# Kernel optimization log

Hardware: AMD Instinct MI355X
Metric: run time of the kernel (lower is better)

Reference implementation:

```python
import jax, jax.numpy as jnp
import numpy as np

B, S, E, H = 2, 2048, 1024, 16
D = E // H  # head_dim = 64


def setup_inputs() -> dict:
    key = jax.random.key(0)
    ks = jax.random.split(key, 6)
    sc = 0.02
    return {
        "hidden_states": jax.random.normal(ks[0], (B, S, E), dtype=jnp.float32),
        "attn_bias": jax.random.normal(ks[1], (S, S), dtype=jnp.float32) * sc,
        "Wqkv": jax.random.normal(ks[2], (E, 3 * E), dtype=jnp.float32) * sc,
        "bqkv": jax.random.normal(ks[3], (3 * E,), dtype=jnp.float32) * sc,
        "Wproj": jax.random.normal(ks[4], (E, E), dtype=jnp.float32) * sc,
        "bproj": jax.random.normal(ks[5], (E,), dtype=jnp.float32) * sc,
    }


def reference(hidden_states, attn_bias, Wqkv, bqkv, Wproj, bproj):
    b, s, e = hidden_states.shape
    qkv = hidden_states @ Wqkv + bqkv                      # [b,s,3e]
    q, k, v = jnp.split(qkv, 3, axis=-1)                   # each [b,s,e]
    cache_key, cache_value = k, v                          # kvCache
    # [b,h,s,d]
    qh = q.reshape(b, s, H, D).transpose(0, 2, 1, 3)
    kh = k.reshape(b, s, H, D).transpose(0, 2, 1, 3)
    vh = v.reshape(b, s, H, D).transpose(0, 2, 1, 3)
    scores = jnp.einsum("bhqd,bhkd->bhqk", qh, kh) / jnp.sqrt(jnp.float32(D))
    scores = scores + attn_bias[:s, :s][None, None]        # learned additive bias
    causal = jnp.tril(jnp.ones((s, s), dtype=bool))
    scores = jnp.where(causal[None, None], scores, jnp.float32(-1e9))
    attn = jax.nn.softmax(scores, axis=-1)
    ctx = jnp.einsum("bhqk,bhkd->bhqd", attn, vh)
    ctx = ctx.transpose(0, 2, 1, 3).reshape(b, s, e)
    out = ctx @ Wproj + bproj                              # resid dropout p=0 -> identity
    return (out, cache_key, cache_value)
```

## Files before the change

kernel.cpp:

```cpp
#include <hip/hip_runtime.h>

#define B_ 2
#define S_ 2048
#define E_ 1024
#define H_ 16
#define D_ 64

typedef short  s16x8 __attribute__((ext_vector_type(8)));
typedef float  f32x4 __attribute__((ext_vector_type(4)));
typedef unsigned short u16x4 __attribute__((ext_vector_type(4)));

__device__ __forceinline__ ushort f2bf(float f) {
    union { float f; unsigned u; } x; x.f = f;
    unsigned u = x.u + 0x7fffu + ((x.u >> 16) & 1u);
    return (ushort)(u >> 16);
}

__device__ __forceinline__ float fast_exp2(float x) {
    float r; asm("v_exp_f32 %0, %1" : "=v"(r) : "v"(x)); return r;
}

__global__ __launch_bounds__(256) void prep_fused_kernel(
    const float* __restrict__ X, ushort* __restrict__ Xbf,
    const float* __restrict__ Wqkv, ushort* __restrict__ Wqkvt,
    const float* __restrict__ Wproj, ushort* __restrict__ Wprojt)
{
    __shared__ float tile[64][65];
    int blk = blockIdx.x;
    int tid = threadIdx.x;
    if (blk < 4096) {
        int i = (blk * 256 + tid) * 4;
        float4 v = *(const float4*)&X[i];
        u16x4 o;
        o.x = f2bf(v.x); o.y = f2bf(v.y); o.z = f2bf(v.z); o.w = f2bf(v.w);
        *(u16x4*)&Xbf[i] = o;
        return;
    }
    const float* W; ushort* Wt; int Ndim, nb;
    if (blk < 4096 + 768) { blk -= 4096; W = Wqkv;  Wt = Wqkvt;  Ndim = 3 * E_; nb = 48; }
    else                  { blk -= 4864; W = Wproj; Wt = Wprojt; Ndim = E_;     nb = 16; }
    int n0 = (blk % nb) * 64, k0 = (blk / nb) * 64;
    int c = tid & 63;
#pragma unroll
    for (int r = tid >> 6; r < 64; r += 4)
        tile[r][c] = W[(size_t)(k0 + r) * Ndim + n0 + c];
    __syncthreads();
#pragma unroll
    for (int r = tid >> 6; r < 64; r += 4)
        Wt[(size_t)(n0 + r) * E_ + k0 + c] = f2bf(tile[c][r]);
}

__global__ __launch_bounds__(256) void prep_bias_kernel(
    const float* __restrict__ bias, ushort* __restrict__ biasT)
{
    int L = blockIdx.x;
    int qi = (int)((sqrtf(8.0f * (float)L + 1.0f) - 1.0f) * 0.5f);
    while ((qi + 1) * (qi + 2) / 2 <= L) qi++;
    while (qi * (qi + 1) / 2 > L) qi--;
    int ki = L - qi * (qi + 1) / 2;
    int tid = threadIdx.x;
    int w = tid >> 6, quad = (tid >> 4) & 3, l15 = tid & 15;
    const float LOG2E = 1.4426950408889634f;
    s16x8 h0 = (s16x8){0,0,0,0,0,0,0,0}, h1 = (s16x8){0,0,0,0,0,0,0,0};
#pragma unroll
    for (int r = 0; r < 4; r++)
#pragma unroll
        for (int kt = 0; kt < 4; kt++) {
            float v = bias[(size_t)(qi * 64 + w * 16 + quad * 4 + r) * S_
                           + ki * 64 + kt * 16 + l15] * LOG2E;
            ushort u = f2bf(v);
            int idx = r * 4 + kt;
            if (idx < 8) h0[idx] = (short)u; else h1[idx - 8] = (short)u;
        }
    ushort* dst = &biasT[((size_t)L * 256 + tid) * 16];
    *(s16x8*)dst = h0;
    *(s16x8*)(dst + 8) = h1;
}

__global__ __launch_bounds__(256) void gemm_mfma_bt(
    const ushort* __restrict__ A,
    const ushort* __restrict__ Bt,
    const float* __restrict__ bias,
    int M, int N, int K,
    float* __restrict__ C0,
    ushort* __restrict__ Qbf, float* __restrict__ Kf32, ushort* __restrict__ Kbf,
    float* __restrict__ Vf32, int mode)
{
    __shared__ ushort As[128 * 64];
    __shared__ ushort Bs[128 * 64];
    int tid = threadIdx.x;
    int wid = tid >> 6, lane = tid & 63;
    int l15 = lane & 15, quad = lane >> 4;
    int wm = wid >> 1, wn = wid & 1;
    int row0 = blockIdx.y * 128, col0 = blockIdx.x * 128;

    int srow = tid >> 3;
    int pk = (tid & 7) * 8;
    int sk = (((tid & 7) ^ (srow & 7)) * 8);

    f32x4 acc[4][4];
#pragma unroll
    for (int mt = 0; mt < 4; mt++)
#pragma unroll
        for (int nt = 0; nt < 4; nt++) acc[mt][nt] = (f32x4){0.f, 0.f, 0.f, 0.f};

    for (int k0 = 0; k0 < K; k0 += 64) {
        __syncthreads();
#pragma unroll
        for (int c = 0; c < 4; c++) {
            int r = c * 32 + srow;
            __builtin_amdgcn_global_load_lds(
                (const __attribute__((address_space(1))) unsigned int*)
                    &A[(size_t)(row0 + r) * K + k0 + sk],
                (__attribute__((address_space(3))) unsigned int*)&As[r * 64 + pk],
                16, 0, 0);
            __builtin_amdgcn_global_load_lds(
                (const __attribute__((address_space(1))) unsigned int*)
                    &Bt[(size_t)(col0 + r) * K + k0 + sk],
                (__attribute__((address_space(3))) unsigned int*)&Bs[r * 64 + pk],
                16, 0, 0);
        }
        __syncthreads();

#pragma unroll
        for (int kk = 0; kk < 2; kk++) {
            int xc = (((kk * 4 + quad) ^ (l15 & 7)) * 8);
            s16x8 af[4], bf[4];
#pragma unroll
            for (int mt = 0; mt < 4; mt++)
                af[mt] = *(const s16x8*)&As[(wm * 64 + mt * 16 + l15) * 64 + xc];
#pragma unroll
            for (int nt = 0; nt < 4; nt++)
                bf[nt] = *(const s16x8*)&Bs[(wn * 64 + nt * 16 + l15) * 64 + xc];
#pragma unroll
            for (int mt = 0; mt < 4; mt++)
#pragma unroll
                for (int nt = 0; nt < 4; nt++)
                    acc[mt][nt] = __builtin_amdgcn_mfma_f32_16x16x32_bf16(
                        af[mt], bf[nt], acc[mt][nt], 0, 0, 0);
        }
    }

#pragma unroll
    for (int nt = 0; nt < 4; nt++) {
        int n = col0 + wn * 64 + nt * 16 + l15;
        float bv = bias[n];
        if (mode == 1) {
            int seg = n >> 10;
            int nn = n & (E_ - 1);
#pragma unroll
            for (int mt = 0; mt < 4; mt++)
#pragma unroll
                for (int r = 0; r < 4; r++) {
                    int row = row0 + wm * 64 + mt * 16 + quad * 4 + r;
                    float v = acc[mt][nt][r] + bv;
                    size_t idx = (size_t)row * E_ + nn;
                    if (seg == 0)      Qbf[idx] = f2bf(v);
                    else if (seg == 1) { Kf32[idx] = v; Kbf[idx] = f2bf(v); }
                    else               Vf32[idx] = v;
                }
        } else {
#pragma unroll
            for (int mt = 0; mt < 4; mt++)
#pragma unroll
                for (int r = 0; r < 4; r++) {
                    int row = row0 + wm * 64 + mt * 16 + quad * 4 + r;
                    C0[(size_t)row * N + n] = acc[mt][nt][r] + bv;
                }
        }
    }
}

__global__ __launch_bounds__(256) void vtrans_kernel(
    const float* __restrict__ V, ushort* __restrict__ Vt)
{
    __shared__ float tile[64][65];
    int blk = blockIdx.x;
    int s0 = (blk & 31) * 64;
    int bh = blk >> 5;
    int b = bh >> 4, h = bh & 15;
    int tid = threadIdx.x;
    int d = tid & 63;
#pragma unroll
    for (int i = tid >> 6; i < 64; i += 4)
        tile[i][d] = V[((size_t)(b * S_ + s0 + i)) * E_ + h * 64 + d];
    __syncthreads();
    int lane = tid & 63, w = tid >> 6;
    int src = ((lane & 3) * 16) + (lane >> 2);
#pragma unroll
    for (int dd = w; dd < 64; dd += 4)
        Vt[((size_t)(bh * 64 + dd)) * S_ + s0 + lane] = f2bf(tile[src][dd]);
}

__global__ __launch_bounds__(256) void attn_mfma_kernel(
    const ushort* __restrict__ Qbf,
    const ushort* __restrict__ Kbf,
    const ushort* __restrict__ Vt,
    const ushort* __restrict__ biasT,
    ushort* __restrict__ Ctx)
{
    __shared__ ushort Ks[64][64];
    __shared__ ushort Vs[64][64];
    __shared__ ushort Ps[4][16][72];

    int blk = blockIdx.x;
    int bh = blk & 31;
    int pr = blk >> 5;
    int b = bh >> 4, h = bh & 15;
    int tid = threadIdx.x;
    int wid = tid >> 6, lane = tid & 63;
    int l15 = lane & 15, quad = lane >> 4;

    int skey = tid >> 2;
    int scol = (tid & 3) * 16;
    int sc0 = ((((tid & 3) * 2) ^ (skey & 7)) * 8);
    int sc1 = sc0 ^ 8;
    const float scale_l2e = 0.18033688011112042f;

    const size_t krow = (size_t)(b * S_ + skey) * E_ + h * 64 + scol;
    const size_t vrow = (size_t)(bh * 64 + skey) * S_ + scol;
    int rc0 = (quad ^ (l15 & 7)) * 8;

    for (int half = 0; half < 2; half++) {
        int qt = half ? pr : (31 - pr);
        int q0w = qt * 64 + wid * 16;

        const size_t qbase = ((size_t)(b * S_ + q0w + l15)) * E_ + h * 64 + quad * 8;
        s16x8 qa0 = *(const s16x8*)&Qbf[qbase];
        s16x8 qa1 = *(const s16x8*)&Qbf[qbase + 32];

        f32x4 o[4];
#pragma unroll
        for (int dt = 0; dt < 4; dt++) o[dt] = (f32x4){0.f, 0.f, 0.f, 0.f};
        float lsum[4];
#pragma unroll
        for (int r = 0; r < 4; r++) lsum[r] = 0.f;

        float4 kr0 = ((const float4*)&Kbf[krow])[0];
        float4 kr1 = ((const float4*)&Kbf[krow])[1];
        float4 vr0 = ((const float4*)&Vt[vrow])[0];
        float4 vr1 = ((const float4*)&Vt[vrow])[1];
        const ushort* bt = &biasT[((size_t)(qt * (qt + 1) / 2) * 256 + tid) * 16];
        s16x8 bn0 = *(const s16x8*)bt;
        s16x8 bn1 = *(const s16x8*)(bt + 8);

        for (int t = 0; t <= qt; t++) {
            int j0 = t * 64;
            __syncthreads();
            *(float4*)&Ks[skey][sc0] = kr0;
            *(float4*)&Ks[skey][sc1] = kr1;
            *(float4*)&Vs[skey][sc0] = vr0;
            *(float4*)&Vs[skey][sc1] = vr1;
            s16x8 b0 = bn0, b1 = bn1;
            __syncthreads();

            if (t < qt) {
                int j1 = j0 + 64;
                kr0 = ((const float4*)&Kbf[krow + (size_t)j1 * E_])[0];
                kr1 = ((const float4*)&Kbf[krow + (size_t)j1 * E_])[1];
                vr0 = ((const float4*)&Vt[vrow + j1])[0];
                vr1 = ((const float4*)&Vt[vrow + j1])[1];
                const ushort* btn = bt + (size_t)(t + 1) * 4096;
                bn0 = *(const s16x8*)btn;
                bn1 = *(const s16x8*)(btn + 8);
            }

            f32x4 s[4];
#pragma unroll
            for (int kt = 0; kt < 4; kt++) {
                s16x8 kb0 = *(const s16x8*)&Ks[kt * 16 + l15][rc0];
                s16x8 kb1 = *(const s16x8*)&Ks[kt * 16 + l15][rc0 ^ 32];
                f32x4 acc = (f32x4){0.f, 0.f, 0.f, 0.f};
                acc = __builtin_amdgcn_mfma_f32_16x16x32_bf16(qa0, kb0, acc, 0, 0, 0);
                acc = __builtin_amdgcn_mfma_f32_16x16x32_bf16(qa1, kb1, acc, 0, 0, 0);
                s[kt] = acc;
            }

            bool diag = (t == qt);
#pragma unroll
            for (int r = 0; r < 4; r++) {
                int row = q0w + quad * 4 + r;
                float pv[4];
#pragma unroll
                for (int kt = 0; kt < 4; kt++) {
                    int j = j0 + kt * 16 + l15;
                    int idx = r * 4 + kt;
                    ushort ub = (ushort)((idx < 8) ? b0[idx] : b1[idx - 8]);
                    union { unsigned u; float f; } bc; bc.u = ((unsigned)ub) << 16;
                    float v = fmaf(s[kt][r], scale_l2e, bc.f);
                    float p = (diag && j > row) ? 0.f : fast_exp2(v);
                    lsum[r] += p;
                    pv[kt] = p;
                }
                unsigned w0, w1;
                asm("v_cvt_pk_bf16_f32 %0, %1, %2" : "=v"(w0) : "v"(pv[0]), "v"(pv[1]));
                asm("v_cvt_pk_bf16_f32 %0, %1, %2" : "=v"(w1) : "v"(pv[2]), "v"(pv[3]));
                uint2 wv; wv.x = w0; wv.y = w1;
                *(uint2*)&Ps[wid][quad * 4 + r][l15 * 4] = wv;
            }

            s16x8 pa0 = *(const s16x8*)&Ps[wid][l15][quad * 8];
            s16x8 pa1 = *(const s16x8*)&Ps[wid][l15][32 + quad * 8];
#pragma unroll
            for (int dt = 0; dt < 4; dt++) {
                s16x8 vb0 = *(const s16x8*)&Vs[dt * 16 + l15][rc0];
                s16x8 vb1 = *(const s16x8*)&Vs[dt * 16 + l15][rc0 ^ 32];
                o[dt] = __builtin_amdgcn_mfma_f32_16x16x32_bf16(pa0, vb0, o[dt], 0, 0, 0);
                o[dt] = __builtin_amdgcn_mfma_f32_16x16x32_bf16(pa1, vb1, o[dt], 0, 0, 0);
            }
        }

        float inv_l[4];
#pragma unroll
        for (int r = 0; r < 4; r++) {
            float l = lsum[r];
            l += __shfl_xor(l, 1);
            l += __shfl_xor(l, 2);
            l += __shfl_xor(l, 4);
            l += __shfl_xor(l, 8);
            inv_l[r] = 1.f / l;
        }

#pragma unroll
        for (int dt = 0; dt < 4; dt++) {
#pragma unroll
            for (int r = 0; r < 4; r++) {
                int row = q0w + quad * 4 + r;
                Ctx[((size_t)(b * S_ + row)) * E_ + h * 64 + dt * 16 + l15] =
                    f2bf(o[dt][r] * inv_l[r]);
            }
        }
    }
}

extern "C" void kernel_launch(void* const* d_in, const int* in_sizes, int n_in,
                              void* d_out, int out_size, void* d_ws, size_t ws_size,
                              hipStream_t stream) {
    const float* X     = (const float*)d_in[0];
    const float* abias = (const float*)d_in[1];
    const float* Wqkv  = (const float*)d_in[2];
    const float* bqkv  = (const float*)d_in[3];
    const float* Wproj = (const float*)d_in[4];
    const float* bproj = (const float*)d_in[5];

    const size_t plane = (size_t)B_ * S_ * E_;
    float* out  = (float*)d_out;
    float* kout = out + plane;
    float* vout = kout + plane;

    ushort* xbf    = (ushort*)d_ws;
    ushort* qbf    = xbf + plane;
    ushort* kbf    = qbf + plane;
    ushort* vt     = kbf + plane;
    ushort* ctxbf  = xbf;
    ushort* wqkvt  = vt + plane;
    ushort* wprojt = wqkvt + (size_t)3 * E_ * E_;
    ushort* biasT  = wqkvt;

    const int M = B_ * S_;

    prep_fused_kernel<<<dim3(5120), 256, 0, stream>>>(
        X, xbf, Wqkv, wqkvt, Wproj, wprojt);

    gemm_mfma_bt<<<dim3(3 * E_ / 128, M / 128), 256, 0, stream>>>(
        xbf, wqkvt, bqkv, M, 3 * E_, E_,
        nullptr, qbf, kout, kbf, vout, 1);

    vtrans_kernel<<<dim3(B_ * H_ * (S_ / 64)), 256, 0, stream>>>(vout, vt);

    prep_bias_kernel<<<dim3(528), 256, 0, stream>>>(abias, biasT);

    attn_mfma_kernel<<<dim3(B_ * H_ * 16), 256, 0, stream>>>(
        qbf, kbf, vt, biasT, ctxbf);

    gemm_mfma_bt<<<dim3(E_ / 128, M / 128), 256, 0, stream>>>(
        ctxbf, wprojt, bproj, M, E_, E_,
        out, nullptr, nullptr, nullptr, nullptr, 0);
}
```

Measured before the change: 214.0 us.

## Double-buffer K/V tiles in attention and merge V-transpose with bias prep

The attention kernel now keeps two LDS buffers for K and V. The next tile is written into the alternate buffer and a tile two steps ahead is prefetched into registers, which cuts the barriers per iteration from two to one. Separately, the V transpose and bias-prep kernels are merged into one launch to save a kernel launch and its tail. LDS use per block roughly doubles for K/V, which may lower occupancy, and register pressure rises from holding prefetches further ahead.

```diff
diff --git a/kernel.cpp b/kernel.cpp
--- a/kernel.cpp
+++ b/kernel.cpp
@@ -50,15 +50,34 @@
         Wt[(size_t)(n0 + r) * E_ + k0 + c] = f2bf(tile[c][r]);
 }
 
-__global__ __launch_bounds__(256) void prep_bias_kernel(
+__global__ __launch_bounds__(256) void post_qkv_kernel(
+    const float* __restrict__ V, ushort* __restrict__ Vt,
     const float* __restrict__ bias, ushort* __restrict__ biasT)
 {
-    int L = blockIdx.x;
+    __shared__ float tile[64][65];
+    int blk = blockIdx.x;
+    int tid = threadIdx.x;
+    if (blk < 1024) {
+        int s0 = (blk & 31) * 64;
+        int bh = blk >> 5;
+        int b = bh >> 4, h = bh & 15;
+        int d = tid & 63;
+#pragma unroll
+        for (int i = tid >> 6; i < 64; i += 4)
+            tile[i][d] = V[((size_t)(b * S_ + s0 + i)) * E_ + h * 64 + d];
+        __syncthreads();
+        int lane = tid & 63, w = tid >> 6;
+        int src = ((lane & 3) * 16) + (lane >> 2);
+#pragma unroll
+        for (int dd = w; dd < 64; dd += 4)
+            Vt[((size_t)(bh * 64 + dd)) * S_ + s0 + lane] = f2bf(tile[src][dd]);
+        return;
+    }
+    int L = blk - 1024;
     int qi = (int)((sqrtf(8.0f * (float)L + 1.0f) - 1.0f) * 0.5f);
     while ((qi + 1) * (qi + 2) / 2 <= L) qi++;
     while (qi * (qi + 1) / 2 > L) qi--;
     int ki = L - qi * (qi + 1) / 2;
-    int tid = threadIdx.x;
     int w = tid >> 6, quad = (tid >> 4) & 3, l15 = tid & 15;
     const float LOG2E = 1.4426950408889634f;
     s16x8 h0 = (s16x8){0,0,0,0,0,0,0,0}, h1 = (s16x8){0,0,0,0,0,0,0,0};
@@ -171,27 +190,6 @@
     }
 }
 
-__global__ __launch_bounds__(256) void vtrans_kernel(
-    const float* __restrict__ V, ushort* __restrict__ Vt)
-{
-    __shared__ float tile[64][65];
-    int blk = blockIdx.x;
-    int s0 = (blk & 31) * 64;
-    int bh = blk >> 5;
-    int b = bh >> 4, h = bh & 15;
-    int tid = threadIdx.x;
-    int d = tid & 63;
-#pragma unroll
-    for (int i = tid >> 6; i < 64; i += 4)
-        tile[i][d] = V[((size_t)(b * S_ + s0 + i)) * E_ + h * 64 + d];
-    __syncthreads();
-    int lane = tid & 63, w = tid >> 6;
-    int src = ((lane & 3) * 16) + (lane >> 2);
-#pragma unroll
-    for (int dd = w; dd < 64; dd += 4)
-        Vt[((size_t)(bh * 64 + dd)) * S_ + s0 + lane] = f2bf(tile[src][dd]);
-}
-
 __global__ __launch_bounds__(256) void attn_mfma_kernel(
     const ushort* __restrict__ Qbf,
     const ushort* __restrict__ Kbf,
@@ -199,8 +197,8 @@
     const ushort* __restrict__ biasT,
     ushort* __restrict__ Ctx)
 {
-    __shared__ ushort Ks[64][64];
-    __shared__ ushort Vs[64][64];
+    __shared__ ushort Ks[2][64][64];
+    __shared__ ushort Vs[2][64][64];
     __shared__ ushort Ps[4][16][72];
 
     int blk = blockIdx.x;
@@ -236,30 +234,47 @@
 #pragma unroll
         for (int r = 0; r < 4; r++) lsum[r] = 0.f;
 
-        float4 kr0 = ((const float4*)&Kbf[krow])[0];
-        float4 kr1 = ((const float4*)&Kbf[krow])[1];
-        float4 vr0 = ((const float4*)&Vt[vrow])[0];
-        float4 vr1 = ((const float4*)&Vt[vrow])[1];
+        {
+            float4 k0a = ((const float4*)&Kbf[krow])[0];
+            float4 k0b = ((const float4*)&Kbf[krow])[1];
+            float4 v0a = ((const float4*)&Vt[vrow])[0];
+            float4 v0b = ((const float4*)&Vt[vrow])[1];
+            *(float4*)&Ks[0][skey][sc0] = k0a;
+            *(float4*)&Ks[0][skey][sc1] = k0b;
+            *(float4*)&Vs[0][skey][sc0] = v0a;
+            *(float4*)&Vs[0][skey][sc1] = v0b;
+        }
+        float4 kr0, kr1, vr0, vr1;
+        if (qt >= 1) {
+            kr0 = ((const float4*)&Kbf[krow + (size_t)64 * E_])[0];
+            kr1 = ((const float4*)&Kbf[krow + (size_t)64 * E_])[1];
+            vr0 = ((const float4*)&Vt[vrow + 64])[0];
+            vr1 = ((const float4*)&Vt[vrow + 64])[1];
+        }
         const ushort* bt = &biasT[((size_t)(qt * (qt + 1) / 2) * 256 + tid) * 16];
         s16x8 bn0 = *(const s16x8*)bt;
         s16x8 bn1 = *(const s16x8*)(bt + 8);
+        __syncthreads();
 
         for (int t = 0; t <= qt; t++) {
             int j0 = t * 64;
-            __syncthreads();
-            *(float4*)&Ks[skey][sc0] = kr0;
-            *(float4*)&Ks[skey][sc1] = kr1;
-            *(float4*)&Vs[skey][sc0] = vr0;
-            *(float4*)&Vs[skey][sc1] = vr1;
+            int cur = t & 1, nxt = cur ^ 1;
+
+            if (t < qt) {
+                *(float4*)&Ks[nxt][skey][sc0] = kr0;
+                *(float4*)&Ks[nxt][skey][sc1] = kr1;
+                *(float4*)&Vs[nxt][skey][sc0] = vr0;
+                *(float4*)&Vs[nxt][skey][sc1] = vr1;
+            }
+            if (t + 2 <= qt) {
+                size_t koff = krow + (size_t)((t + 2) * 64) * E_;
+                kr0 = ((const float4*)&Kbf[koff])[0];
+                kr1 = ((const float4*)&Kbf[koff])[1];
+                vr0 = ((const float4*)&Vt[vrow + (t + 2) * 64])[0];
+                vr1 = ((const float4*)&Vt[vrow + (t + 2) * 64])[1];
+            }
             s16x8 b0 = bn0, b1 = bn1;
-            __syncthreads();
-
             if (t < qt) {
-                int j1 = j0 + 64;
-                kr0 = ((const float4*)&Kbf[krow + (size_t)j1 * E_])[0];
-                kr1 = ((const float4*)&Kbf[krow + (size_t)j1 * E_])[1];
-                vr0 = ((const float4*)&Vt[vrow + j1])[0];
-                vr1 = ((const float4*)&Vt[vrow + j1])[1];
                 const ushort* btn = bt + (size_t)(t + 1) * 4096;
                 bn0 = *(const s16x8*)btn;
                 bn1 = *(const s16x8*)(btn + 8);
@@ -268,8 +283,8 @@
             f32x4 s[4];
 #pragma unroll
             for (int kt = 0; kt < 4; kt++) {
-                s16x8 kb0 = *(const s16x8*)&Ks[kt * 16 + l15][rc0];
-                s16x8 kb1 = *(const s16x8*)&Ks[kt * 16 + l15][rc0 ^ 32];
+                s16x8 kb0 = *(const s16x8*)&Ks[cur][kt * 16 + l15][rc0];
+                s16x8 kb1 = *(const s16x8*)&Ks[cur][kt * 16 + l15][rc0 ^ 32];
                 f32x4 acc = (f32x4){0.f, 0.f, 0.f, 0.f};
                 acc = __builtin_amdgcn_mfma_f32_16x16x32_bf16(qa0, kb0, acc, 0, 0, 0);
                 acc = __builtin_amdgcn_mfma_f32_16x16x32_bf16(qa1, kb1, acc, 0, 0, 0);
@@ -303,11 +318,13 @@
             s16x8 pa1 = *(const s16x8*)&Ps[wid][l15][32 + quad * 8];
 #pragma unroll
             for (int dt = 0; dt < 4; dt++) {
-                s16x8 vb0 = *(const s16x8*)&Vs[dt * 16 + l15][rc0];
-                s16x8 vb1 = *(const s16x8*)&Vs[dt * 16 + l15][rc0 ^ 32];
+                s16x8 vb0 = *(const s16x8*)&Vs[cur][dt * 16 + l15][rc0];
+                s16x8 vb1 = *(const s16x8*)&Vs[cur][dt * 16 + l15][rc0 ^ 32];
                 o[dt] = __builtin_amdgcn_mfma_f32_16x16x32_bf16(pa0, vb0, o[dt], 0, 0, 0);
                 o[dt] = __builtin_amdgcn_mfma_f32_16x16x32_bf16(pa1, vb1, o[dt], 0, 0, 0);
             }
+
+            __syncthreads();
         }
 
         float inv_l[4];
@@ -366,9 +383,8 @@
         xbf, wqkvt, bqkv, M, 3 * E_, E_,
         nullptr, qbf, kout, kbf, vout, 1);
 
-    vtrans_kernel<<<dim3(B_ * H_ * (S_ / 64)), 256, 0, stream>>>(vout, vt);
-
-    prep_bias_kernel<<<dim3(528), 256, 0, stream>>>(abias, biasT);
+    post_qkv_kernel<<<dim3(1024 + 528), 256, 0, stream>>>(
+        vout, vt, abias, biasT);
 
     attn_mfma_kernel<<<dim3(B_ * H_ * 16), 256, 0, stream>>>(
         qbf, kbf, vt, biasT, ctxbf);
```

Measured after the change: 211.8 us. About the same (-1.1%).

## Compute transposed scores to keep P in registers and merge prep kernels

Applied to the files above, without the earlier changes.

The QK^T MFMA operands are swapped so each lane holds a column slice of scores that maps directly onto the A-operand layout of the PV MFMA. This removes the per-wave LDS round trip for the probability tile. The V-transpose permutation and the bias-reordering layout are changed to match, and the row sum is reduced with fewer shuffles. The V transpose and bias prep kernels are fused into one launch, saving a kernel launch. The risk is that the new index mappings for bias and Vt must line up exactly with the new fragment layout.

```diff
diff --git a/kernel.cpp b/kernel.cpp
--- a/kernel.cpp
+++ b/kernel.cpp
@@ -50,28 +50,54 @@
         Wt[(size_t)(n0 + r) * E_ + k0 + c] = f2bf(tile[c][r]);
 }
 
-__global__ __launch_bounds__(256) void prep_bias_kernel(
+__global__ __launch_bounds__(256) void post_qkv_kernel(
+    const float* __restrict__ V, ushort* __restrict__ Vt,
     const float* __restrict__ bias, ushort* __restrict__ biasT)
 {
-    int L = blockIdx.x;
+    __shared__ float tile[64][65];
+    int blk = blockIdx.x;
+    int tid = threadIdx.x;
+    if (blk < 1024) {
+        int s0 = (blk & 31) * 64;
+        int bh = blk >> 5;
+        int b = bh >> 4, h = bh & 15;
+        int d = tid & 63;
+#pragma unroll
+        for (int i = tid >> 6; i < 64; i += 4)
+            tile[i][d] = V[((size_t)(b * S_ + s0 + i)) * E_ + h * 64 + d];
+        __syncthreads();
+        int lane = tid & 63, w = tid >> 6;
+        int g = lane >> 5, rem = lane & 31, q2 = rem >> 3, i2 = rem & 7;
+        int src = (2 * g + (i2 >> 2)) * 16 + q2 * 4 + (i2 & 3);
+#pragma unroll
+        for (int dd = w; dd < 64; dd += 4)
+            Vt[((size_t)(bh * 64 + dd)) * S_ + s0 + lane] = f2bf(tile[src][dd]);
+        return;
+    }
+    int L = blk - 1024;
     int qi = (int)((sqrtf(8.0f * (float)L + 1.0f) - 1.0f) * 0.5f);
     while ((qi + 1) * (qi + 2) / 2 <= L) qi++;
     while (qi * (qi + 1) / 2 > L) qi--;
     int ki = L - qi * (qi + 1) / 2;
-    int tid = threadIdx.x;
     int w = tid >> 6, quad = (tid >> 4) & 3, l15 = tid & 15;
     const float LOG2E = 1.4426950408889634f;
     s16x8 h0 = (s16x8){0,0,0,0,0,0,0,0}, h1 = (s16x8){0,0,0,0,0,0,0,0};
 #pragma unroll
-    for (int r = 0; r < 4; r++)
-#pragma unroll
-        for (int kt = 0; kt < 4; kt++) {
-            float v = bias[(size_t)(qi * 64 + w * 16 + quad * 4 + r) * S_
-                           + ki * 64 + kt * 16 + l15] * LOG2E;
-            ushort u = f2bf(v);
-            int idx = r * 4 + kt;
-            if (idx < 8) h0[idx] = (short)u; else h1[idx - 8] = (short)u;
-        }
+    for (int kt = 0; kt < 4; kt++) {
+        float4 v4 = *(const float4*)&bias[(size_t)(qi * 64 + w * 16 + l15) * S_
+                                          + ki * 64 + kt * 16 + quad * 4];
+        ushort u0 = f2bf(v4.x * LOG2E);
+        ushort u1 = f2bf(v4.y * LOG2E);
+        ushort u2 = f2bf(v4.z * LOG2E);
+        ushort u3 = f2bf(v4.w * LOG2E);
+        if (kt < 2) {
+            h0[kt * 4 + 0] = (short)u0; h0[kt * 4 + 1] = (short)u1;
+            h0[kt * 4 + 2] = (short)u2; h0[kt * 4 + 3] = (short)u3;
+        } else {
+            h1[(kt - 2) * 4 + 0] = (short)u0; h1[(kt - 2) * 4 + 1] = (short)u1;
+            h1[(kt - 2) * 4 + 2] = (short)u2; h1[(kt - 2) * 4 + 3] = (short)u3;
+        }
+    }
     ushort* dst = &biasT[((size_t)L * 256 + tid) * 16];
     *(s16x8*)dst = h0;
     *(s16x8*)(dst + 8) = h1;
@@ -171,27 +197,6 @@
     }
 }
 
-__global__ __launch_bounds__(256) void vtrans_kernel(
-    const float* __restrict__ V, ushort* __restrict__ Vt)
-{
-    __shared__ float tile[64][65];
-    int blk = blockIdx.x;
-    int s0 = (blk & 31) * 64;
-    int bh = blk >> 5;
-    int b = bh >> 4, h = bh & 15;
-    int tid = threadIdx.x;
-    int d = tid & 63;
-#pragma unroll
-    for (int i = tid >> 6; i < 64; i += 4)
-        tile[i][d] = V[((size_t)(b * S_ + s0 + i)) * E_ + h * 64 + d];
-    __syncthreads();
-    int lane = tid & 63, w = tid >> 6;
-    int src = ((lane & 3) * 16) + (lane >> 2);
-#pragma unroll
-    for (int dd = w; dd < 64; dd += 4)
-        Vt[((size_t)(bh * 64 + dd)) * S_ + s0 + lane] = f2bf(tile[src][dd]);
-}
-
 __global__ __launch_bounds__(256) void attn_mfma_kernel(
     const ushort* __restrict__ Qbf,
     const ushort* __restrict__ Kbf,
@@ -201,7 +206,6 @@
 {
     __shared__ ushort Ks[64][64];
     __shared__ ushort Vs[64][64];
-    __shared__ ushort Ps[4][16][72];
 
     int blk = blockIdx.x;
     int bh = blk & 31;
@@ -224,6 +228,7 @@
     for (int half = 0; half < 2; half++) {
         int qt = half ? pr : (31 - pr);
         int q0w = qt * 64 + wid * 16;
+        int rowq = q0w + l15;
 
         const size_t qbase = ((size_t)(b * S_ + q0w + l15)) * E_ + h * 64 + quad * 8;
         s16x8 qa0 = *(const s16x8*)&Qbf[qbase];
@@ -232,9 +237,7 @@
         f32x4 o[4];
 #pragma unroll
         for (int dt = 0; dt < 4; dt++) o[dt] = (f32x4){0.f, 0.f, 0.f, 0.f};
-        float lsum[4];
-#pragma unroll
-        for (int r = 0; r < 4; r++) lsum[r] = 0.f;
+        float ls = 0.f;
 
         float4 kr0 = ((const float4*)&Kbf[krow])[0];
         float4 kr1 = ((const float4*)&Kbf[krow])[1];
@@ -271,36 +274,37 @@
                 s16x8 kb0 = *(const s16x8*)&Ks[kt * 16 + l15][rc0];
                 s16x8 kb1 = *(const s16x8*)&Ks[kt * 16 + l15][rc0 ^ 32];
                 f32x4 acc = (f32x4){0.f, 0.f, 0.f, 0.f};
-                acc = __builtin_amdgcn_mfma_f32_16x16x32_bf16(qa0, kb0, acc, 0, 0, 0);
-                acc = __builtin_amdgcn_mfma_f32_16x16x32_bf16(qa1, kb1, acc, 0, 0, 0);
+                acc = __builtin_amdgcn_mfma_f32_16x16x32_bf16(kb0, qa0, acc, 0, 0, 0);
+                acc = __builtin_amdgcn_mfma_f32_16x16x32_bf16(kb1, qa1, acc, 0, 0, 0);
                 s[kt] = acc;
             }
 
             bool diag = (t == qt);
-#pragma unroll
-            for (int r = 0; r < 4; r++) {
-                int row = q0w + quad * 4 + r;
+            unsigned upk[8];
+#pragma unroll
+            for (int kt = 0; kt < 4; kt++) {
                 float pv[4];
 #pragma unroll
-                for (int kt = 0; kt < 4; kt++) {
-                    int j = j0 + kt * 16 + l15;
-                    int idx = r * 4 + kt;
+                for (int r = 0; r < 4; r++) {
+                    int idx = kt * 4 + r;
                     ushort ub = (ushort)((idx < 8) ? b0[idx] : b1[idx - 8]);
                     union { unsigned u; float f; } bc; bc.u = ((unsigned)ub) << 16;
                     float v = fmaf(s[kt][r], scale_l2e, bc.f);
-                    float p = (diag && j > row) ? 0.f : fast_exp2(v);
-                    lsum[r] += p;
-                    pv[kt] = p;
+                    int j = j0 + kt * 16 + quad * 4 + r;
+                    float p = (diag && j > rowq) ? 0.f : fast_exp2(v);
+                    ls += p;
+                    pv[r] = p;
                 }
-                unsigned w0, w1;
-                asm("v_cvt_pk_bf16_f32 %0, %1, %2" : "=v"(w0) : "v"(pv[0]), "v"(pv[1]));
-                asm("v_cvt_pk_bf16_f32 %0, %1, %2" : "=v"(w1) : "v"(pv[2]), "v"(pv[3]));
-                uint2 wv; wv.x = w0; wv.y = w1;
-                *(uint2*)&Ps[wid][quad * 4 + r][l15 * 4] = wv;
-            }
-
-            s16x8 pa0 = *(const s16x8*)&Ps[wid][l15][quad * 8];
-            s16x8 pa1 = *(const s16x8*)&Ps[wid][l15][32 + quad * 8];
+                asm("v_cvt_pk_bf16_f32 %0, %1, %2"
+                    : "=v"(upk[kt * 2]) : "v"(pv[0]), "v"(pv[1]));
+                asm("v_cvt_pk_bf16_f32 %0, %1, %2"
+                    : "=v"(upk[kt * 2 + 1]) : "v"(pv[2]), "v"(pv[3]));
+            }
+            uint4 ua = make_uint4(upk[0], upk[1], upk[2], upk[3]);
+            uint4 ub4 = make_uint4(upk[4], upk[5], upk[6], upk[7]);
+            s16x8 pa0 = *(s16x8*)&ua;
+            s16x8 pa1 = *(s16x8*)&ub4;
+
 #pragma unroll
             for (int dt = 0; dt < 4; dt++) {
                 s16x8 vb0 = *(const s16x8*)&Vs[dt * 16 + l15][rc0];
@@ -310,16 +314,14 @@
             }
         }
 
+        float l = ls;
+        l += __shfl_xor(l, 16);
+        l += __shfl_xor(l, 32);
+        float inv = 1.f / l;
         float inv_l[4];
 #pragma unroll
-        for (int r = 0; r < 4; r++) {
-            float l = lsum[r];
-            l += __shfl_xor(l, 1);
-            l += __shfl_xor(l, 2);
-            l += __shfl_xor(l, 4);
-            l += __shfl_xor(l, 8);
-            inv_l[r] = 1.f / l;
-        }
+        for (int r = 0; r < 4; r++)
+            inv_l[r] = __shfl(inv, quad * 4 + r);
 
 #pragma unroll
         for (int dt = 0; dt < 4; dt++) {
@@ -366,9 +368,8 @@
         xbf, wqkvt, bqkv, M, 3 * E_, E_,
         nullptr, qbf, kout, kbf, vout, 1);
 
-    vtrans_kernel<<<dim3(B_ * H_ * (S_ / 64)), 256, 0, stream>>>(vout, vt);
-
-    prep_bias_kernel<<<dim3(528), 256, 0, stream>>>(abias, biasT);
+    post_qkv_kernel<<<dim3(1024 + 528), 256, 0, stream>>>(
+        vout, vt, abias, biasT);
 
     attn_mfma_kernel<<<dim3(B_ * H_ * 16), 256, 0, stream>>>(
         qbf, kbf, vt, biasT, ctxbf);
```

New measurement: 214.6 us. Within noise of the previous version (+0.3%).
